# Performance work log

Measured on AMD Instinct MI355X. Metric: run time of the kernel, lower is better.

## Reference

```python
import jax, jax.numpy as jnp
import numpy as np

K = 3      # spline order
NUM = 5    # grid intervals


def bspline_basis(x, grid, k=K):
    """Cox-de Boor recursion. x: (B, D); grid: (num+2k+1,) extended knots.
    Returns basis of shape (B, D, num+k)."""
    xe = x[..., None]                                       # (B, D, 1)
    B = ((xe >= grid[:-1]) & (xe < grid[1:])).astype(x.dtype)  # (B, D, num+2k)
    for p in range(1, k + 1):
        left = (xe - grid[:-(p + 1)]) / (grid[p:-1] - grid[:-(p + 1)])
        right = (grid[p + 1:] - xe) / (grid[p + 1:] - grid[1:-p])
        B = left * B[..., :-1] + right * B[..., 1:]
    return B                                                # (B, D, num+k)


def kan_layer(x, grid, coef, sb, sp, mask, bias):
    """phi(x)[b,o] = sum_i mask[o,i]*(sb[o,i]*silu(x[b,i]) + sp[o,i]*sum_c B[b,i,c]*coef[o,i,c]) + bias[o]"""
    Bsp = bspline_basis(x, grid)                            # (B, in, C)
    spline = jnp.einsum('bic,oic->bo', Bsp, coef * (sp * mask)[:, :, None])
    base = jnp.einsum('bi,oi->bo', jax.nn.silu(x), sb * mask)
    return base + spline + bias


def setup_inputs() -> dict:
    key = jax.random.key(0)
    ks = jax.random.split(key, 6)
    Bch, d0, d1, d2 = 8192, 1024, 2048, 1024
    C = NUM + K                                 # 8 spline coeffs per edge
    h = 2.0 / NUM                               # grid_range [-1,1]
    # extended knot vector: k extra knots each side, num+2k+1 = 12 points
    grid = jnp.arange(-K, NUM + K + 1, dtype=jnp.float32) * h - 1.0
    return {
        "x": jax.random.normal(ks[0], (Bch, d0), jnp.float32) * 0.5,
        "coef0": jax.random.normal(ks[1], (d1, d0, C), jnp.float32) * 0.1,
        "sb0": jax.random.normal(ks[2], (d1, d0), jnp.float32) / np.sqrt(d0).astype(np.float32),
        "sp0": jnp.ones((d1, d0), jnp.float32),
        "mask0": jnp.ones((d1, d0), jnp.float32),
        "bias0": jnp.zeros((d1,), jnp.float32),
        "coef1": jax.random.normal(ks[3], (d2, d1, C), jnp.float32) * 0.1,
        "sb1": jax.random.normal(ks[4], (d2, d1), jnp.float32) / np.sqrt(d1).astype(np.float32),
        "sp1": jnp.ones((d2, d1), jnp.float32),
        "mask1": jnp.ones((d2, d1), jnp.float32),
        "bias1": jnp.zeros((d2,), jnp.float32),
        "grid": grid,
    }


def reference(x, coef0, sb0, sp0, mask0, bias0, coef1, sb1, sp1, mask1, bias1, grid):
    h1 = kan_layer(x, grid, coef0, sb0, sp0, mask0, bias0)
    out = kan_layer(h1, grid, coef1, sb1, sp1, mask1, bias1)
    return out
```

## Files before the change

### kernel.cpp

```cpp
#include <hip/hip_runtime.h>
#include <hip/hip_bf16.h>
#include <cstdint>


typedef __attribute__((ext_vector_type(8))) short short8;
typedef __attribute__((ext_vector_type(4))) short short4v;
typedef __attribute__((ext_vector_type(4))) float f32x4;

#define GLD16(gp, lp)                                                          \
  __builtin_amdgcn_global_load_lds(                                           \
      (const __attribute__((address_space(1))) unsigned int*)(gp),             \
      (__attribute__((address_space(3))) unsigned int*)(lp), 16, 0, 0)

__device__ __forceinline__ unsigned short f2bf(float f) {
  __hip_bfloat16 h = __float2bfloat16(f);
  return *reinterpret_cast<unsigned short*>(&h);
}

__device__ __forceinline__ void basis8(float x, float* w, int& j) {
  float u  = (x + 2.2f) * 2.5f;
  float fj = floorf(u);
  j = (int)fj;
  float t  = u - fj;
  float omt = 1.0f - t;
  float t2 = t * t, t3 = t2 * t;
  w[0] = omt * omt * omt * (1.0f / 6.0f);
  w[1] = (3.0f * t3 - 6.0f * t2 + 4.0f) * (1.0f / 6.0f);
  w[2] = (-3.0f * t3 + 3.0f * t2 + 3.0f * t + 1.0f) * (1.0f / 6.0f);
  w[3] = t3 * (1.0f / 6.0f);
}

__device__ __forceinline__ void prep_w_item(
    long idx, const float* __restrict__ coef, const float* __restrict__ sb,
    const float* __restrict__ sp, const float* __restrict__ mask,
    __hip_bfloat16* __restrict__ W, int I) {
  int qtr = I >> 2;
  int iq = (int)(idx % qtr);
  int o  = (int)(idx / qtr);
  int i  = iq << 2;
  size_t oi = (size_t)o * I + i;
  float4 mk4 = *(const float4*)(mask + oi);
  float4 sp4 = *(const float4*)(sp + oi);
  float4 sb4 = *(const float4*)(sb + oi);
  float spm[4] = {sp4.x * mk4.x, sp4.y * mk4.y, sp4.z * mk4.z, sp4.w * mk4.w};
  float cf[4][8];
  const float4* cp = (const float4*)(coef + oi * 8);
#pragma unroll
  for (int e = 0; e < 4; e++) {
    float4 a = cp[e * 2], b = cp[e * 2 + 1];
    cf[e][0] = a.x; cf[e][1] = a.y; cf[e][2] = a.z; cf[e][3] = a.w;
    cf[e][4] = b.x; cf[e][5] = b.y; cf[e][6] = b.z; cf[e][7] = b.w;
  }
  __hip_bfloat16* base = W + (size_t)o * (size_t)(9 * I) + (i >> 6) * 576 + (i & 63);
#pragma unroll
  for (int c = 0; c < 8; c++) {
    short4v pk;
#pragma unroll
    for (int e = 0; e < 4; e++) pk[e] = (short)f2bf(cf[e][c] * spm[e]);
    *(short4v*)(base + c * 64) = pk;
  }
  short4v ps;
  ps[0] = (short)f2bf(sb4.x * mk4.x); ps[1] = (short)f2bf(sb4.y * mk4.y);
  ps[2] = (short)f2bf(sb4.z * mk4.z); ps[3] = (short)f2bf(sb4.w * mk4.w);
  *(short4v*)(base + 8 * 64) = ps;
}

__device__ __forceinline__ void expand_item(
    long idx, const float* __restrict__ src, __hip_bfloat16* __restrict__ aug,
    int I) {
  int  oct = I >> 3;
  int  io = (int)(idx % oct);
  long b  = idx / oct;
  int  i  = io << 3;
  const float* sp = src + b * (size_t)I + i;
  float4 xa = *(const float4*)sp;
  float4 xb = *(const float4*)(sp + 4);
  float xv[8] = {xa.x, xa.y, xa.z, xa.w, xb.x, xb.y, xb.z, xb.w};

  float w[8][4], s[8];
  int   j[8];
#pragma unroll
  for (int e = 0; e < 8; e++) {
    float xe = xv[e];
    s[e] = xe / (1.0f + __expf(-xe));
    basis8(xe, w[e], j[e]);
  }
  __hip_bfloat16* base = aug + b * (size_t)(9 * I) + (i >> 6) * 576 + (i & 63);
#pragma unroll
  for (int c = 0; c < 8; c++) {
    short8 pk;
#pragma unroll
    for (int e = 0; e < 8; e++) {
      int d = j[e] - c;
      float v = 0.0f;
      v = (d == 0) ? w[e][3] : v;
      v = (d == 1) ? w[e][2] : v;
      v = (d == 2) ? w[e][1] : v;
      v = (d == 3) ? w[e][0] : v;
      pk[e] = (short)f2bf(v);
    }
    *(short8*)(base + c * 64) = pk;
  }
  short8 ps;
#pragma unroll
  for (int e = 0; e < 8; e++) ps[e] = (short)f2bf(s[e]);
  *(short8*)(base + 8 * 64) = ps;
}

__global__ void prep_merge(
    const float* __restrict__ coef, const float* __restrict__ sb,
    const float* __restrict__ sp, const float* __restrict__ mask,
    __hip_bfloat16* __restrict__ W, int IW, long nW,
    const float* __restrict__ xsrc, __hip_bfloat16* __restrict__ aug,
    int IX, long nX) {
  long idx = (long)blockIdx.x * blockDim.x + threadIdx.x;
  if (idx < nW)            prep_w_item(idx, coef, sb, sp, mask, W, IW);
  else if (idx < nW + nX)  expand_item(idx - nW, xsrc, aug, IX);
}

__global__ void expand_aug(const float* __restrict__ src,
                           __hip_bfloat16* __restrict__ aug,
                           long totalOcts, int I) {
  long idx = (long)blockIdx.x * blockDim.x + threadIdx.x;
  if (idx >= totalOcts) return;
  expand_item(idx, src, aug, I);
}

template <int BN>
__global__ __launch_bounds__(512, 4) void gemm128(
    const __hip_bfloat16* __restrict__ A, const __hip_bfloat16* __restrict__ Bw,
    const float* __restrict__ bias, float* __restrict__ Cout, int N, int K) {
  constexpr int WN   = BN / 4;
  constexpr int NREP = BN / 64;
  constexpr int BUFB = 8192 + BN * 64;
  __shared__ __attribute__((aligned(16))) char lds[3 * BUFB];

  const int t = threadIdx.x;
  const int w = t >> 6, l = t & 63;
  const int wr = w >> 2, wc = w & 3;
  const int lr = l & 15;
  const int kbs = ((l >> 4) * 16) ^ (((lr >> 1) & 3) << 4);

  unsigned nwg = gridDim.x * gridDim.y;
  unsigned lin = blockIdx.y * gridDim.x + blockIdx.x;
  unsigned swz = (lin & 7) * (nwg >> 3) + (lin >> 3);
  unsigned bx = swz % gridDim.x, by = swz / gridDim.x;
  size_t brow = (size_t)by * 128, bcol = (size_t)bx * BN;

  f32x4 acc[4][NREP];
#pragma unroll
  for (int m = 0; m < 4; m++)
#pragma unroll
    for (int n = 0; n < NREP; n++) acc[m][n] = (f32x4){0.f, 0.f, 0.f, 0.f};

  const int srow  = t >> 2;
  const int scolb = ((t & 3) * 16) ^ (((srow >> 1) & 3) << 4);
  const __hip_bfloat16* gA0 = A + (brow + srow) * (size_t)K + (scolb >> 1);
  const __hip_bfloat16* gB0 = Bw + (bcol + srow) * (size_t)K + (scolb >> 1);
  const __hip_bfloat16* gB1 = gB0 + (size_t)128 * K;

  char* ldsp = (char*)lds;
  const int paOff = (wr * 64 + lr) * 64 + kbs;
  const int pbOff = 8192 + (wc * WN + lr) * 64 + kbs;

  auto STAGE = [&](int kt, int q) {
    char* bp = ldsp + q * BUFB;
    GLD16(gA0 + (kt << 5), bp + w * 1024);
    GLD16(gB0 + (kt << 5), bp + 8192 + w * 1024);
    if constexpr (BN == 256) GLD16(gB1 + (kt << 5), bp + 16384 + w * 1024);
  };
  auto COMPUTE = [&](int q) {
    const char* pa = ldsp + q * BUFB + paOff;
    const char* pb = ldsp + q * BUFB + pbOff;
    short8 bq[NREP], aq[4];
#pragma unroll
    for (int n = 0; n < NREP; n++) bq[n] = *(const short8*)(pb + n * 1024);
#pragma unroll
    for (int m = 0; m < 4; m++) aq[m] = *(const short8*)(pa + m * 1024);
    __builtin_amdgcn_s_setprio(1);
#pragma unroll
    for (int m = 0; m < 4; m++)
#pragma unroll
      for (int n = 0; n < NREP; n++)
        acc[m][n] = __builtin_amdgcn_mfma_f32_16x16x32_bf16(aq[m], bq[n], acc[m][n], 0, 0, 0);
    __builtin_amdgcn_s_setprio(0);
    __builtin_amdgcn_s_barrier();
  };
  auto VM0 = [&]() { asm volatile("s_waitcnt vmcnt(0)" ::: "memory"); };
  auto VML = [&]() {
    if constexpr (BN == 256) asm volatile("s_waitcnt vmcnt(3)" ::: "memory");
    else                     asm volatile("s_waitcnt vmcnt(2)" ::: "memory");
  };
  auto VM2L = [&]() {
    if constexpr (BN == 256) asm volatile("s_waitcnt vmcnt(6)" ::: "memory");
    else                     asm volatile("s_waitcnt vmcnt(4)" ::: "memory");
  };

  const int NT = K >> 5;

  STAGE(0, 0);
  STAGE(1, 1);
  VML();
  __builtin_amdgcn_s_barrier();

  int q0 = 0;
  for (int kt = 0; kt < NT - 2; ++kt) {
    int q2 = q0 + 2; if (q2 >= 3) q2 -= 3;
    STAGE(kt + 2, q2);
    VM2L();
    __builtin_amdgcn_s_barrier();
    COMPUTE(q0);
    q0 = (q0 == 2) ? 0 : q0 + 1;
  }
  VML();
  __builtin_amdgcn_s_barrier();
  COMPUTE(q0);
  q0 = (q0 == 2) ? 0 : q0 + 1;
  VM0();
  __builtin_amdgcn_s_barrier();
  COMPUTE(q0);

  const int orow = (l >> 4) << 2;
#pragma unroll
  for (int n = 0; n < NREP; n++) {
    size_t col = bcol + (size_t)wc * WN + n * 16 + lr;
    float bv = bias[col];
#pragma unroll
    for (int m = 0; m < 4; m++) {
      size_t row = brow + (size_t)wr * 64 + m * 16 + orow;
#pragma unroll
      for (int r = 0; r < 4; r++)
        Cout[(row + r) * (size_t)N + col] = acc[m][n][r] + bv;
    }
  }
}

extern "C" void kernel_launch(void* const* d_in, const int* in_sizes, int n_in,
                              void* d_out, int out_size, void* d_ws, size_t ws_size,
                              hipStream_t stream) {
  const float* x     = (const float*)d_in[0];
  const float* coef0 = (const float*)d_in[1];
  const float* sb0   = (const float*)d_in[2];
  const float* sp0   = (const float*)d_in[3];
  const float* mask0 = (const float*)d_in[4];
  const float* bias0 = (const float*)d_in[5];
  const float* coef1 = (const float*)d_in[6];
  const float* sb1   = (const float*)d_in[7];
  const float* sp1   = (const float*)d_in[8];
  const float* mask1 = (const float*)d_in[9];
  const float* bias1 = (const float*)d_in[10];
  float* out = (float*)d_out;

  const int B = 8192, D0 = 1024, D1 = 2048, D2 = 1024;
  const int K0 = 9 * D0;
  const int K1 = 9 * D1;
  const int CH = 4096;

  char* ws = (char*)d_ws;
  float*          h1  = (float*)ws;
  __hip_bfloat16* W   = (__hip_bfloat16*)(ws + (size_t)67108864);
  __hip_bfloat16* Aug = (__hip_bfloat16*)(ws + (size_t)104857600);

  const long nW0 = (long)D1 * (D0 / 4);
  const long nX0 = (long)B * (D0 / 8);
  const long nW1 = (long)D2 * (D1 / 4);
  const long nX1 = (long)CH * (D1 / 8);

  prep_merge<<<(unsigned)((nW0 + nX0) / 256), 256, 0, stream>>>(
      coef0, sb0, sp0, mask0, W, D0, nW0, x, Aug, D0, nX0);
  {
    dim3 g0(D1 / 256, B / 128);
    gemm128<256><<<g0, 512, 0, stream>>>(Aug, W, bias0, h1, D1, K0);
  }

  prep_merge<<<(unsigned)((nW1 + nX1) / 256), 256, 0, stream>>>(
      coef1, sb1, sp1, mask1, W, D1, nW1, h1, Aug, D1, nX1);
  {
    dim3 g1(D2 / 128, CH / 128);
    gemm128<128><<<g1, 512, 0, stream>>>(Aug, W, bias1, out, D2, K1);
  }
  expand_aug<<<(unsigned)(nX1 / 256), 256, 0, stream>>>(
      h1 + (size_t)CH * D1, Aug, nX1, D1);
  {
    dim3 g1(D2 / 128, CH / 128);
    gemm128<128><<<g1, 512, 0, stream>>>(Aug, W, bias1,
                                         out + (size_t)CH * D2, D2, K1);
  }
}
```

Before: 789.9 us.

## Use 128x64-tile GEMM with triple-buffered LDS for second-layer GEMMs

Adds a new GEMM kernel with a 128x64 output tile, K-step of 32, and a three-stage LDS ring buffer, and uses it for the two second-layer GEMMs instead of the 128x128 kernel. Each wave computes only four 16x16 MFMA tiles, which lowers register use and LDS footprint and permits four blocks per CU. The aim is more workgroups and better latency hiding for the narrower N=1024 GEMMs. In exchange, each MFMA does less work per LDS load, and B-tile loads are duplicated across the two halves of the workgroup.

```diff
diff --git a/kernel.cpp b/kernel.cpp
--- a/kernel.cpp
+++ b/kernel.cpp
@@ -235,6 +235,96 @@
   }
 }
 
+__global__ __launch_bounds__(512, 4) void gemm64n(
+    const __hip_bfloat16* __restrict__ A, const __hip_bfloat16* __restrict__ Bw,
+    const float* __restrict__ bias, float* __restrict__ Cout, int N, int K) {
+  constexpr int BUFB = 8192 + 4096;
+  __shared__ __attribute__((aligned(16))) char lds[3 * BUFB];
+
+  const int t = threadIdx.x;
+  const int w = t >> 6, l = t & 63;
+  const int wr = w >> 2, wc = w & 3;
+  const int lr = l & 15;
+  const int kbs = ((l >> 4) * 16) ^ (((lr >> 1) & 3) << 4);
+
+  unsigned nwg = gridDim.x * gridDim.y;
+  unsigned lin = blockIdx.y * gridDim.x + blockIdx.x;
+  unsigned swz = (lin & 7) * (nwg >> 3) + (lin >> 3);
+  unsigned bx = swz % gridDim.x, by = swz / gridDim.x;
+  size_t brow = (size_t)by * 128, bcol = (size_t)bx * 64;
+
+  f32x4 acc[4];
+#pragma unroll
+  for (int m = 0; m < 4; m++) acc[m] = (f32x4){0.f, 0.f, 0.f, 0.f};
+
+  const int srow  = t >> 2;
+  const int scolb = ((t & 3) * 16) ^ (((srow >> 1) & 3) << 4);
+  const __hip_bfloat16* gA0 = A + (brow + srow) * (size_t)K + (scolb >> 1);
+  const int tb  = t & 255;
+  const int srB = tb >> 2;
+  const int scB = ((tb & 3) * 16) ^ (((srB >> 1) & 3) << 4);
+  const __hip_bfloat16* gB0 = Bw + (bcol + srB) * (size_t)K + (scB >> 1);
+
+  char* ldsp = (char*)lds;
+  const int paOff = (wr * 64 + lr) * 64 + kbs;
+  const int pbOff = 8192 + (wc * 16 + lr) * 64 + kbs;
+
+  auto STAGE = [&](int kt, int q) {
+    char* bp = ldsp + q * BUFB;
+    GLD16(gA0 + (kt << 5), bp + w * 1024);
+    GLD16(gB0 + (kt << 5), bp + 8192 + (w & 3) * 1024);
+  };
+  auto COMPUTE = [&](int q) {
+    const char* pa = ldsp + q * BUFB + paOff;
+    const char* pb = ldsp + q * BUFB + pbOff;
+    short8 bq = *(const short8*)pb;
+    short8 aq[4];
+#pragma unroll
+    for (int m = 0; m < 4; m++) aq[m] = *(const short8*)(pa + m * 1024);
+    __builtin_amdgcn_s_setprio(1);
+#pragma unroll
+    for (int m = 0; m < 4; m++)
+      acc[m] = __builtin_amdgcn_mfma_f32_16x16x32_bf16(aq[m], bq, acc[m], 0, 0, 0);
+    __builtin_amdgcn_s_setprio(0);
+    __builtin_amdgcn_s_barrier();
+  };
+
+  const int NT = K >> 5;
+
+  STAGE(0, 0);
+  STAGE(1, 1);
+  asm volatile("s_waitcnt vmcnt(2)" ::: "memory");
+  __builtin_amdgcn_s_barrier();
+
+  int q0 = 0;
+  for (int kt = 0; kt < NT - 2; ++kt) {
+    int q2 = q0 + 2; if (q2 >= 3) q2 -= 3;
+    STAGE(kt + 2, q2);
+    asm volatile("s_waitcnt vmcnt(4)" ::: "memory");
+    __builtin_amdgcn_s_barrier();
+    COMPUTE(q0);
+    q0 = (q0 == 2) ? 0 : q0 + 1;
+  }
+  asm volatile("s_waitcnt vmcnt(2)" ::: "memory");
+  __builtin_amdgcn_s_barrier();
+  COMPUTE(q0);
+  q0 = (q0 == 2) ? 0 : q0 + 1;
+  asm volatile("s_waitcnt vmcnt(0)" ::: "memory");
+  __builtin_amdgcn_s_barrier();
+  COMPUTE(q0);
+
+  const int orow = (l >> 4) << 2;
+  size_t col = bcol + (size_t)wc * 16 + lr;
+  float bv = bias[col];
+#pragma unroll
+  for (int m = 0; m < 4; m++) {
+    size_t row = brow + (size_t)wr * 64 + m * 16 + orow;
+#pragma unroll
+    for (int r = 0; r < 4; r++)
+      Cout[(row + r) * (size_t)N + col] = acc[m][r] + bv;
+  }
+}
+
 extern "C" void kernel_launch(void* const* d_in, const int* in_sizes, int n_in,
                               void* d_out, int out_size, void* d_ws, size_t ws_size,
                               hipStream_t stream) {
@@ -276,14 +366,14 @@
   prep_merge<<<(unsigned)((nW1 + nX1) / 256), 256, 0, stream>>>(
       coef1, sb1, sp1, mask1, W, D1, nW1, h1, Aug, D1, nX1);
   {
-    dim3 g1(D2 / 128, CH / 128);
-    gemm128<128><<<g1, 512, 0, stream>>>(Aug, W, bias1, out, D2, K1);
+    dim3 g1(D2 / 64, CH / 128);
+    gemm64n<<<g1, 512, 0, stream>>>(Aug, W, bias1, out, D2, K1);
   }
   expand_aug<<<(unsigned)(nX1 / 256), 256, 0, stream>>>(
       h1 + (size_t)CH * D1, Aug, nX1, D1);
   {
-    dim3 g1(D2 / 128, CH / 128);
-    gemm128<128><<<g1, 512, 0, stream>>>(Aug, W, bias1,
-                                         out + (size_t)CH * D2, D2, K1);
-  }
-}
+    dim3 g1(D2 / 64, CH / 128);
+    gemm64n<<<g1, 512, 0, stream>>>(Aug, W, bias1,
+                                    out + (size_t)CH * D2, D2, K1);
+  }
+}
```

After: 955.9 us. 21.0% more time.
